# Kernel tuning notes

Hardware: AMD Instinct MI355X
Metric: run time of the kernel (lower is better)

Reference implementation:

```python
import jax, jax.numpy as jnp
import numpy as np

N = 300000   # active voxels at level 1
P = 150000   # indice pairs per kernel offset
K = 27       # 3x3x3 submanifold kernel offsets
C = 32       # nPlanes[0] = m
M = N // 8   # output voxels after stride-2 downsample
P2 = N       # stride-conv pairs for downsample
EPS = 1e-4   # BatchNorm1d eps in Semantic


def setup_inputs() -> dict:
    key = jax.random.key(0)
    ks = jax.random.split(key, 8)
    feats = jax.random.normal(ks[0], (N, C), jnp.float32)
    xyz = jax.random.normal(ks[1], (N, 3), jnp.float32)
    batch = jax.random.randint(ks[2], (N,), 0, 4)
    pair_in = jax.random.randint(ks[3], (K, P), 0, N)
    pair_out = jax.random.randint(ks[4], (K, P), 0, N)
    valid = jax.random.bernoulli(ks[5], 0.9, (K, P))
    pair_in = jnp.where(valid, pair_in, -1)  # spconv pads unused pairs with -1
    ds_pair_in = jax.random.randint(ks[6], (P2,), 0, N)
    ds_pair_out = jax.random.randint(ks[7], (P2,), 0, M)
    kw = jax.random.split(jax.random.key(1), 2)
    std = 1.0 / np.sqrt(C * K)
    W1 = jax.random.normal(kw[0], (K, C, C), jnp.float32) * std
    W2 = jax.random.normal(kw[1], (K, C, C), jnp.float32) * std
    return dict(feats=feats, xyz=xyz, batch=batch, pair_in=pair_in,
                pair_out=pair_out, ds_pair_in=ds_pair_in,
                ds_pair_out=ds_pair_out, W1=W1, W2=W2)


def bn_relu(x):
    # BatchNorm1d in train mode with weight=1, bias=0 (set_bn_init), then ReLU
    mu = jnp.mean(x, axis=0)
    var = jnp.var(x, axis=0)
    return jax.nn.relu((x - mu) * jax.lax.rsqrt(var + EPS))


def submconv(x, W, pair_in, pair_out):
    # gather-GEMM-scatter submanifold conv: x [N,Ci], W [K,Ci,Co], pairs [K,P]
    valid = pair_in >= 0
    gath = x[jnp.where(valid, pair_in, 0)]                 # [K,P,Ci]
    contrib = jnp.einsum('kpc,kcd->kpd', gath, W)          # [K,P,Co]
    seg = jnp.where(valid, pair_out, N).reshape(-1)        # invalid -> dump slot N
    out = jax.ops.segment_sum(contrib.reshape(-1, W.shape[-1]), seg,
                              num_segments=N + 1)
    return out[:N]


def scatter_mean(vals, idx_in, idx_out, num_out):
    valid = idx_in >= 0
    v = vals[jnp.where(valid, idx_in, 0)]
    v = jnp.where(valid[:, None], v, 0.0) if v.ndim == 2 else jnp.where(valid, v, 0.0)
    seg = jnp.where(valid, idx_out, num_out)
    sums = jax.ops.segment_sum(v, seg, num_segments=num_out + 1)[:num_out]
    cnt = jax.ops.segment_sum(valid.astype(jnp.float32), seg,
                              num_segments=num_out + 1)[:num_out]
    cnt = jnp.maximum(cnt, 1.0)
    return sums / (cnt[:, None] if sums.ndim == 2 else cnt)


def reference(feats, xyz, batch, pair_in, pair_out, ds_pair_in, ds_pair_out, W1, W2):
    # ResidualBlock: norm->relu->subm3x3 -> norm->relu->subm3x3, identity add
    h = submconv(bn_relu(feats), W1, pair_in, pair_out)
    h = submconv(bn_relu(h), W2, pair_in, pair_out)
    out = h + feats
    # get_downsample_info: scatter_mean of xyz and batch over stride-conv pairs
    xyz_next = scatter_mean(xyz, ds_pair_in, ds_pair_out, M)
    batch_next = scatter_mean(batch.astype(jnp.float32), ds_pair_in, ds_pair_out, M)
    return out, xyz_next, batch_next
```

## Files before the change

### kernel.cpp

```cpp
#include <hip/hip_runtime.h>

#define BN_EPS 1e-4f
#define BKT_SH 8
#define NBUCK_MAX 2560
#define CBLK 1024
#define LDSCAP 4096
#define P3CAP 4096

typedef __attribute__((ext_vector_type(8))) short short8;
typedef __attribute__((ext_vector_type(4))) float f32x4;
typedef __attribute__((ext_vector_type(4))) float floatv4;
typedef unsigned int uint;

union U4S8 { uint4 u; short8 s; };

static __device__ __forceinline__ unsigned short f2bf(float f) {
    unsigned u = __float_as_uint(f);
    unsigned r = (u + 0x7FFFu + ((u >> 16) & 1u)) >> 16;
    return (unsigned short)r;
}

__global__ void stats_bf16(const ushort* __restrict__ x,
                           float* __restrict__ stats, int n8) {
    const int t = threadIdx.x;
    long idx = (long)blockIdx.x * 256 + t;
    const long stride = (long)gridDim.x * 256;
    float s[8] = {0}, q[8] = {0};
    const uint4* x8 = (const uint4*)x;
    for (long e = idx; e < n8; e += stride) {
        uint4 v = x8[e];
        uint w0 = v.x, w1 = v.y, w2 = v.z, w3 = v.w;
        float f0 = __uint_as_float(w0 << 16), f1 = __uint_as_float(w0 & 0xFFFF0000u);
        float f2 = __uint_as_float(w1 << 16), f3 = __uint_as_float(w1 & 0xFFFF0000u);
        float f4 = __uint_as_float(w2 << 16), f5 = __uint_as_float(w2 & 0xFFFF0000u);
        float f6 = __uint_as_float(w3 << 16), f7 = __uint_as_float(w3 & 0xFFFF0000u);
        s[0]+=f0; q[0]+=f0*f0; s[1]+=f1; q[1]+=f1*f1;
        s[2]+=f2; q[2]+=f2*f2; s[3]+=f3; q[3]+=f3*f3;
        s[4]+=f4; q[4]+=f4*f4; s[5]+=f5; q[5]+=f5*f5;
        s[6]+=f6; q[6]+=f6*f6; s[7]+=f7; q[7]+=f7*f7;
    }
    __shared__ float red[256][8];
#pragma unroll
    for (int j = 0; j < 8; ++j) red[t][j] = s[j];
    __syncthreads();
    if (t < 32) {
        float a = 0.f;
        const int grp = t >> 3, j = t & 7;
#pragma unroll
        for (int m = 0; m < 64; ++m) a += red[grp + 4 * m][j];
        atomicAdd(&stats[t], a);
    }
    __syncthreads();
#pragma unroll
    for (int j = 0; j < 8; ++j) red[t][j] = q[j];
    __syncthreads();
    if (t < 32) {
        float a = 0.f;
        const int grp = t >> 3, j = t & 7;
#pragma unroll
        for (int m = 0; m < 64; ++m) a += red[grp + 4 * m][j];
        atomicAdd(&stats[32 + t], a);
    }
}

__global__ void bnrelu_f32(const float* __restrict__ x,
                           const float* __restrict__ stats,
                           ushort* __restrict__ xb, int n8, int N) {
    int idx = blockIdx.x * 256 + threadIdx.x;
    if (idx >= n8) return;
    const int c0 = (idx & 3) * 8;
    const float invN = 1.0f / (float)N;
    floatv4 v0 = *(const floatv4*)(x + (size_t)idx * 8);
    floatv4 v1 = *(const floatv4*)(x + (size_t)idx * 8 + 4);
    uint r[8];
#pragma unroll
    for (int j = 0; j < 8; ++j) {
        const int c = c0 + j;
        float mu = stats[c] * invN;
        float var = stats[32 + c] * invN - mu * mu;
        float rs = rsqrtf(var + BN_EPS);
        float f = (j < 4) ? v0[j] : v1[j - 4];
        float xn = fmaxf((f - mu) * rs, 0.f);
        r[j] = (uint)f2bf(xn);
    }
    uint4 o;
    o.x = r[0] | (r[1] << 16); o.y = r[2] | (r[3] << 16);
    o.z = r[4] | (r[5] << 16); o.w = r[6] | (r[7] << 16);
    *(uint4*)(xb + (size_t)idx * 8) = o;
}

__global__ void bnrelu_bf16(const ushort* __restrict__ h,
                            const float* __restrict__ stats,
                            ushort* __restrict__ xb, int n8, int N) {
    int idx = blockIdx.x * 256 + threadIdx.x;
    if (idx >= n8) return;
    const int c0 = (idx & 3) * 8;
    const float invN = 1.0f / (float)N;
    uint4 v = *(const uint4*)(h + (size_t)idx * 8);
    uint w[4] = {v.x, v.y, v.z, v.w};
    uint r[8];
#pragma unroll
    for (int j = 0; j < 8; ++j) {
        const int c = c0 + j;
        float mu = stats[c] * invN;
        float var = stats[32 + c] * invN - mu * mu;
        float rs = rsqrtf(var + BN_EPS);
        uint bits = (j & 1) ? (w[j >> 1] & 0xFFFF0000u) : (w[j >> 1] << 16);
        float f = __uint_as_float(bits);
        float xn = fmaxf((f - mu) * rs, 0.f);
        r[j] = (uint)f2bf(xn);
    }
    uint4 o;
    o.x = r[0] | (r[1] << 16); o.y = r[2] | (r[3] << 16);
    o.z = r[4] | (r[5] << 16); o.w = r[6] | (r[7] << 16);
    *(uint4*)(xb + (size_t)idx * 8) = o;
}

__global__ void prep2(const float* __restrict__ W1, const float* __restrict__ W2,
                      ushort* __restrict__ Wt1, ushort* __restrict__ Wt2,
                      ushort* __restrict__ xb,
                      const float* __restrict__ xyz, const int* __restrict__ batch,
                      floatv4* __restrict__ xyzb, int N, int B0,
                      const float* __restrict__ feats, float* __restrict__ stats1,
                      int total4) {
    const int t = threadIdx.x;
    if ((int)blockIdx.x >= B0) {
        const int bid = blockIdx.x - B0;
        long idx = (long)bid * 256 + t;
        const long stride = 1024L * 256;
        float s[4] = {0.f, 0.f, 0.f, 0.f}, q[4] = {0.f, 0.f, 0.f, 0.f};
        const floatv4* x4 = (const floatv4*)feats;
        for (long e = idx; e < total4; e += stride) {
            floatv4 v = x4[e];
#pragma unroll
            for (int j = 0; j < 4; ++j) { s[j] += v[j]; q[j] += v[j] * v[j]; }
        }
        __shared__ float red[256][4];
#pragma unroll
        for (int j = 0; j < 4; ++j) red[t][j] = s[j];
        __syncthreads();
        if (t < 32) {
            float a = 0.f;
            const int grp = t >> 2, j = t & 3;
#pragma unroll
            for (int m = 0; m < 32; ++m) a += red[grp + 8 * m][j];
            atomicAdd(&stats1[t], a);
        }
        __syncthreads();
#pragma unroll
        for (int j = 0; j < 4; ++j) red[t][j] = q[j];
        __syncthreads();
        if (t < 32) {
            float a = 0.f;
            const int grp = t >> 2, j = t & 3;
#pragma unroll
            for (int m = 0; m < 32; ++m) a += red[grp + 8 * m][j];
            atomicAdd(&stats1[32 + t], a);
        }
        return;
    }
    int idx = blockIdx.x * 256 + t;
    if (idx < 27 * 1024) {
        int k = idx >> 10, r = idx & 1023, co = r >> 5, ci = r & 31;
        Wt1[(k << 10) + (co << 5) + ci] = f2bf(W1[(k << 10) + (ci << 5) + co]);
    } else if (idx < 2 * 27 * 1024) {
        int i2 = idx - 27 * 1024;
        int k = i2 >> 10, r = i2 & 1023, co = r >> 5, ci = r & 31;
        Wt2[(k << 10) + (co << 5) + ci] = f2bf(W2[(k << 10) + (ci << 5) + co]);
    } else if (idx < 2 * 27 * 1024 + 32) {
        xb[(size_t)N * 32 + (idx - 2 * 27 * 1024)] = 0;
    } else {
        int i = idx - (2 * 27 * 1024 + 32);
        if (i < N) {
            floatv4 v;
            v[0] = xyz[(size_t)i * 3 + 0];
            v[1] = xyz[(size_t)i * 3 + 1];
            v[2] = xyz[(size_t)i * 3 + 2];
            v[3] = (float)batch[i];
            xyzb[i] = v;
        }
    }
}


__global__ void p1_count2(const int* __restrict__ pinA, const int* __restrict__ poutA,
                          uint* __restrict__ cntmatA, int KPA, int chunkA, int nbuckA,
                          const int* __restrict__ pinB, const int* __restrict__ poutB,
                          uint* __restrict__ cntmatB, int KPB, int chunkB, int nbuckB) {
    __shared__ uint H[NBUCK_MAX];
    const int t = threadIdx.x;
    const bool isA = (blockIdx.x < CBLK);
    const int j = isA ? blockIdx.x : (blockIdx.x - CBLK);
    const int* pin = isA ? pinA : pinB;
    const int* pout = isA ? poutA : poutB;
    uint* cntmat = isA ? cntmatA : cntmatB;
    const int KP = isA ? KPA : KPB;
    const int chunk = isA ? chunkA : chunkB;
    const int nbuck = isA ? nbuckA : nbuckB;
    for (int i = t; i < nbuck; i += 256) H[i] = 0;
    __syncthreads();
    const int r0 = j * chunk;
    const int r1 = min(KP, r0 + chunk);
    for (int r = r0 + t; r < r1; r += 256)
        if (pin[r] >= 0) atomicAdd(&H[((uint)pout[r]) >> BKT_SH], 1u);
    __syncthreads();
    uint* row = cntmat + (size_t)j * nbuck;
    for (int i = t; i < nbuck; i += 256) row[i] = H[i];
}

__global__ void p2_colscan2(uint* __restrict__ cntmatA, uint* __restrict__ btotA,
                            int nbuckA, int nblkA,
                            uint* __restrict__ cntmatB, uint* __restrict__ btotB,
                            int nbuckB) {
    const bool isA = ((int)blockIdx.x < nblkA);
    const int blk = isA ? blockIdx.x : (blockIdx.x - nblkA);
    uint* cntmat = isA ? cntmatA : cntmatB;
    uint* btot = isA ? btotA : btotB;
    const int nbuck = isA ? nbuckA : nbuckB;
    const int tid = threadIdx.x;
    const int bi  = tid & 15;
    const int seg = tid >> 4;
    const int b   = blk * 16 + bi;
    const int rpseg = CBLK / 16;
    const bool valid = (b < nbuck);
    uint s = 0;
    if (valid) {
        for (int u = 0; u < rpseg; ++u)
            s += cntmat[(size_t)(seg * rpseg + u) * nbuck + b];
    }
    __shared__ uint ss[16][16];
    ss[seg][bi] = s;
    __syncthreads();
    uint pre = 0;
    for (int g = 0; g < seg; ++g) pre += ss[g][bi];
    if (valid && seg == 15) btot[b] = pre + s;
    if (valid) {
        uint run = pre;
        for (int u = 0; u < rpseg; ++u) {
            size_t idx = (size_t)(seg * rpseg + u) * nbuck + b;
            uint v = cntmat[idx];
            cntmat[idx] = run;
            run += v;
        }
    }
}

__global__ void p3_bucketscan2(const uint* __restrict__ btotA, uint* __restrict__ bbaseA,
                               uint* __restrict__ startsA, int nbuckA, int NA,
                               const uint* __restrict__ btotB, uint* __restrict__ bbaseB,
                               uint* __restrict__ startsB, int nbuckB, int NB) {
    const uint* btot; uint* bbase; uint* starts; int nbuck; int N;
    if (blockIdx.x == 0) { btot = btotA; bbase = bbaseA; starts = startsA; nbuck = nbuckA; N = NA; }
    else                 { btot = btotB; bbase = bbaseB; starts = startsB; nbuck = nbuckB; N = NB; }
    const int t = threadIdx.x;
    __shared__ uint part[256];
    uint loc[10]; uint s = 0;
#pragma unroll
    for (int u = 0; u < 10; ++u) {
        int i = t * 10 + u;
        loc[u] = (i < nbuck) ? btot[i] : 0;
        s += loc[u];
    }
    part[t] = s;
    __syncthreads();
    for (int off = 1; off < 256; off <<= 1) {
        uint y = (t >= off) ? part[t - off] : 0;
        __syncthreads();
        part[t] += y;
        __syncthreads();
    }
    uint run = part[t] - s;
#pragma unroll
    for (int u = 0; u < 10; ++u) {
        int i = t * 10 + u;
        if (i < nbuck) { bbase[i] = run; run += loc[u]; }
    }
    if (t == 255) { bbase[nbuck] = run; starts[N] = run; }
}

__global__ __launch_bounds__(256)
void p4_place2(const int* __restrict__ pinA, const int* __restrict__ poutA,
               const uint* __restrict__ cntmatA, const uint* __restrict__ bbaseA,
               uint* __restrict__ tmpA, int KPA, int PA, int chunkA, int nbuckA,
               const int* __restrict__ pinB, const int* __restrict__ poutB,
               const uint* __restrict__ cntmatB, const uint* __restrict__ bbaseB,
               uint* __restrict__ tmpB, int KPB, int PB, int chunkB, int nbuckB) {
    __shared__ uint recs[LDSCAP];
    __shared__ ushort bof[LDSCAP];
    __shared__ uint H[NBUCK_MAX + 1];
    __shared__ uint C[NBUCK_MAX];
    __shared__ uint part[256];
    const int t = threadIdx.x;
    const bool isA = (blockIdx.x < CBLK);
    const int j = isA ? blockIdx.x : (blockIdx.x - CBLK);
    const int* pin = isA ? pinA : pinB;
    const int* pout = isA ? poutA : poutB;
    const uint* cntmat = isA ? cntmatA : cntmatB;
    const uint* bbase = isA ? bbaseA : bbaseB;
    uint* tmp = isA ? tmpA : tmpB;
    const int KP = isA ? KPA : KPB;
    const int P = isA ? PA : PB;
    const int chunk = isA ? chunkA : chunkB;
    const int nbuck = isA ? nbuckA : nbuckB;
    for (int i = t; i < nbuck; i += 256) H[i] = 0;
    __syncthreads();
    const int r0 = j * chunk;
    const int r1 = min(KP, r0 + chunk);
    for (int r = r0 + t; r < r1; r += 256)
        if (pin[r] >= 0) atomicAdd(&H[((uint)pout[r]) >> BKT_SH], 1u);
    __syncthreads();
    uint loc[10]; uint s = 0;
#pragma unroll
    for (int u = 0; u < 10; ++u) {
        int i = t * 10 + u;
        loc[u] = (i < nbuck) ? H[i] : 0;
        s += loc[u];
    }
    __syncthreads();
    part[t] = s;
    __syncthreads();
    for (int off = 1; off < 256; off <<= 1) {
        uint y = (t >= off) ? part[t - off] : 0;
        __syncthreads();
        part[t] += y;
        __syncthreads();
    }
    uint run = part[t] - s;
#pragma unroll
    for (int u = 0; u < 10; ++u) {
        int i = t * 10 + u;
        if (i < nbuck) { uint c = loc[u]; H[i] = run; run += c; }
    }
    if (t == 255) H[nbuck] = run;
    __syncthreads();
    for (int i = t; i < nbuck; i += 256) C[i] = H[i];
    __syncthreads();
    for (int r = r0 + t; r < r1; r += 256) {
        int ii = pin[r];
        if (ii < 0) continue;
        uint po = (uint)pout[r];
        uint b = po >> BKT_SH;
        uint k = (uint)r / (uint)P;
        uint pos = atomicAdd(&C[b], 1u);
        recs[pos] = ((po & 255u) << 24) | (k << 19) | (uint)ii;
        bof[pos] = (ushort)b;
    }
    __syncthreads();
    const uint tot = H[nbuck];
    for (int i = t; i < nbuck; i += 256)
        C[i] = bbase[i] + cntmat[(size_t)j * nbuck + i] - H[i];
    __syncthreads();
    for (uint sdx = t; sdx < tot; sdx += 256) {
        uint b = (uint)bof[sdx];
        tmp[C[b] + sdx] = recs[sdx];
    }
}

__global__ void p5_fine2(const uint* tmpA, const uint* __restrict__ bbaseA,
                         uint* entriesA, uint* __restrict__ startsA, int NA, int nbuckA,
                         const uint* tmpB, const uint* __restrict__ bbaseB,
                         uint* entriesB, uint* __restrict__ startsB, int NB) {
    __shared__ uint recs[P3CAP];
    __shared__ uint cnt[256];
    __shared__ uint curl[256];
    const bool isA = ((int)blockIdx.x < nbuckA);
    const int b = isA ? blockIdx.x : (blockIdx.x - nbuckA);
    const uint* tmp = isA ? tmpA : tmpB;
    const uint* bbase = isA ? bbaseA : bbaseB;
    uint* entries = isA ? entriesA : entriesB;
    uint* starts = isA ? startsA : startsB;
    const int N = isA ? NA : NB;
    const int t = threadIdx.x;
    const uint e0 = bbase[b];
    uint nrec = bbase[b + 1] - e0;
    if (nrec > P3CAP) nrec = P3CAP;
    for (uint s = t; s < nrec; s += 256) recs[s] = tmp[e0 + s];
    cnt[t] = 0; curl[t] = 0;
    __syncthreads();
    for (uint s = t; s < nrec; s += 256) atomicAdd(&cnt[recs[s] >> 24], 1u);
    __syncthreads();
    uint orig = cnt[t];
    for (int off = 1; off < 256; off <<= 1) {
        uint y = (t >= off) ? cnt[t - off] : 0;
        __syncthreads();
        cnt[t] += y;
        __syncthreads();
    }
    cnt[t] -= orig;
    __syncthreads();
    const int o0 = b << BKT_SH;
    if (o0 + t < N) starts[o0 + t] = e0 + cnt[t];
    for (uint s = t; s < nrec; s += 256) {
        uint lo = recs[s] >> 24;
        uint idx = atomicAdd(&curl[lo], 1u);
        entries[e0 + cnt[lo] + idx] = recs[s] & 0x00FFFFFFu;
    }
}

__global__ void conv1_csr(const ushort* __restrict__ xb,
                          const ushort* __restrict__ Wt,
                          const uint* __restrict__ starts,
                          const uint* __restrict__ entries,
                          ushort* __restrict__ outb,
                          int N) {
    const int w  = threadIdx.x >> 6;
    const int l  = threadIdx.x & 63;
    const int m  = l & 15;
    const int iq = l >> 4;
    const int o0 = (blockIdx.x * 4 + w) * 16;

    __shared__ uint eld[4][384];
    if (o0 >= N) return;

    const uint s0 = starts[o0];
    const uint sm = starts[o0 + m];
    const uint se = starts[o0 + m + 1];
    uint total = starts[o0 + 16] - s0;
    if (total > 384) total = 384;
    for (uint t = l; t < total; t += 64)
        eld[w][t] = entries[s0 + t];
    asm volatile("s_waitcnt lgkmcnt(0) vmcnt(0)" ::: "memory");
    __builtin_amdgcn_sched_barrier(0);

    if (iq == 0) {
        const uint a = sm - s0, bnd = se - s0;
        for (uint i = a + 1; i < bnd; ++i) {
            uint key = eld[w][i];
            uint j = i;
            while (j > a && eld[w][j - 1] > key) { eld[w][j] = eld[w][j - 1]; --j; }
            eld[w][j] = key;
        }
    }
    asm volatile("s_waitcnt lgkmcnt(0)" ::: "memory");
    __builtin_amdgcn_sched_barrier(0);

    f32x4 c0 = {0.f, 0.f, 0.f, 0.f};
    f32x4 c1 = {0.f, 0.f, 0.f, 0.f};
    uint q = sm - s0;
    const uint e = se - s0;
    uint ent = (q < e) ? eld[w][q] : 0xFFFFFFFFu;

    for (int k = 0; k < 27; ++k) {
        const ushort* wk = Wt + (k << 10);
        U4S8 b0, b1;
        b0.u = *(const uint4*)(wk + m * 32 + iq * 8);
        b1.u = *(const uint4*)(wk + (m + 16) * 32 + iq * 8);
        float a0=0.f,a1=0.f,a2=0.f,a3=0.f,a4=0.f,a5=0.f,a6=0.f,a7=0.f;
        bool got = false;
        while ((ent >> 19) == (uint)k) {
            got = true;
            const uint pi = ent & 0x7FFFFu;
            uint4 v = *(const uint4*)(xb + (size_t)pi * 32 + iq * 8);
            a0 += __uint_as_float(v.x << 16);
            a1 += __uint_as_float(v.x & 0xFFFF0000u);
            a2 += __uint_as_float(v.y << 16);
            a3 += __uint_as_float(v.y & 0xFFFF0000u);
            a4 += __uint_as_float(v.z << 16);
            a5 += __uint_as_float(v.z & 0xFFFF0000u);
            a6 += __uint_as_float(v.w << 16);
            a7 += __uint_as_float(v.w & 0xFFFF0000u);
            ++q;
            ent = (q < e) ? eld[w][q] : 0xFFFFFFFFu;
        }
        if (__any(got)) {
            U4S8 af;
            asm volatile("v_cvt_pk_bf16_f32 %0, %1, %2" : "=v"(af.u.x) : "v"(a0), "v"(a1));
            asm volatile("v_cvt_pk_bf16_f32 %0, %1, %2" : "=v"(af.u.y) : "v"(a2), "v"(a3));
            asm volatile("v_cvt_pk_bf16_f32 %0, %1, %2" : "=v"(af.u.z) : "v"(a4), "v"(a5));
            asm volatile("v_cvt_pk_bf16_f32 %0, %1, %2" : "=v"(af.u.w) : "v"(a6), "v"(a7));
            c0 = __builtin_amdgcn_mfma_f32_16x16x32_bf16(af.s, b0.s, c0, 0, 0, 0);
            c1 = __builtin_amdgcn_mfma_f32_16x16x32_bf16(af.s, b1.s, c1, 0, 0, 0);
        }
    }

#pragma unroll
    for (int j = 0; j < 4; ++j) {
        const long ro = (long)(o0 + iq * 4 + j) * 32;
        outb[ro + m]      = f2bf(c0[j]);
        outb[ro + 16 + m] = f2bf(c1[j]);
    }
}

__global__ void conv2_fused(const ushort* __restrict__ xb,
                            const ushort* __restrict__ Wt,
                            const uint* __restrict__ starts,
                            const uint* __restrict__ entries,
                            const float* __restrict__ iden,
                            float* __restrict__ outf,
                            int N, int cblocks,
                            const floatv4* __restrict__ xyzb,
                            const uint* __restrict__ starts2,
                            const uint* __restrict__ entries2,
                            float* __restrict__ out_xyz,
                            float* __restrict__ out_batch, int M) {
    if ((int)blockIdx.x >= cblocks) {
        int o = (blockIdx.x - cblocks) * 256 + threadIdx.x;
        if (o >= M) return;
        const uint s = starts2[o], e = starts2[o + 1];
        float sx = 0.f, sy = 0.f, sz = 0.f, sb = 0.f;
        for (uint q = s; q < e; ++q) {
            uint i = entries2[q] & 0x00FFFFFFu;
            floatv4 v = xyzb[i];
            sx += v[0]; sy += v[1]; sz += v[2]; sb += v[3];
        }
        float c = fmaxf((float)(e - s), 1.0f);
        float inv = 1.0f / c;
        out_xyz[(long)o * 3 + 0] = sx * inv;
        out_xyz[(long)o * 3 + 1] = sy * inv;
        out_xyz[(long)o * 3 + 2] = sz * inv;
        out_batch[o] = sb * inv;
        return;
    }
    const int w  = threadIdx.x >> 6;
    const int l  = threadIdx.x & 63;
    const int m  = l & 15;
    const int iq = l >> 4;
    const int o0 = (blockIdx.x * 4 + w) * 16;

    __shared__ uint eld[4][384];
    if (o0 >= N) return;

    const uint s0 = starts[o0];
    const uint sm = starts[o0 + m];
    const uint se = starts[o0 + m + 1];
    uint total = starts[o0 + 16] - s0;
    if (total > 384) total = 384;
    for (uint t = l; t < total; t += 64)
        eld[w][t] = entries[s0 + t];
    asm volatile("s_waitcnt lgkmcnt(0) vmcnt(0)" ::: "memory");
    __builtin_amdgcn_sched_barrier(0);

    if (iq == 0) {
        const uint a = sm - s0, bnd = se - s0;
        for (uint i = a + 1; i < bnd; ++i) {
            uint key = eld[w][i];
            uint j = i;
            while (j > a && eld[w][j - 1] > key) { eld[w][j] = eld[w][j - 1]; --j; }
            eld[w][j] = key;
        }
    }
    asm volatile("s_waitcnt lgkmcnt(0)" ::: "memory");
    __builtin_amdgcn_sched_barrier(0);

    f32x4 c0 = {0.f, 0.f, 0.f, 0.f};
    f32x4 c1 = {0.f, 0.f, 0.f, 0.f};
    uint q = sm - s0;
    const uint e = se - s0;
    uint ent = (q < e) ? eld[w][q] : 0xFFFFFFFFu;

    for (int k = 0; k < 27; ++k) {
        const ushort* wk = Wt + (k << 10);
        U4S8 b0, b1;
        b0.u = *(const uint4*)(wk + m * 32 + iq * 8);
        b1.u = *(const uint4*)(wk + (m + 16) * 32 + iq * 8);
        float a0=0.f,a1=0.f,a2=0.f,a3=0.f,a4=0.f,a5=0.f,a6=0.f,a7=0.f;
        bool got = false;
        while ((ent >> 19) == (uint)k) {
            got = true;
            const uint pi = ent & 0x7FFFFu;
            uint4 v = *(const uint4*)(xb + (size_t)pi * 32 + iq * 8);
            a0 += __uint_as_float(v.x << 16);
            a1 += __uint_as_float(v.x & 0xFFFF0000u);
            a2 += __uint_as_float(v.y << 16);
            a3 += __uint_as_float(v.y & 0xFFFF0000u);
            a4 += __uint_as_float(v.z << 16);
            a5 += __uint_as_float(v.z & 0xFFFF0000u);
            a6 += __uint_as_float(v.w << 16);
            a7 += __uint_as_float(v.w & 0xFFFF0000u);
            ++q;
            ent = (q < e) ? eld[w][q] : 0xFFFFFFFFu;
        }
        if (__any(got)) {
            U4S8 af;
            asm volatile("v_cvt_pk_bf16_f32 %0, %1, %2" : "=v"(af.u.x) : "v"(a0), "v"(a1));
            asm volatile("v_cvt_pk_bf16_f32 %0, %1, %2" : "=v"(af.u.y) : "v"(a2), "v"(a3));
            asm volatile("v_cvt_pk_bf16_f32 %0, %1, %2" : "=v"(af.u.z) : "v"(a4), "v"(a5));
            asm volatile("v_cvt_pk_bf16_f32 %0, %1, %2" : "=v"(af.u.w) : "v"(a6), "v"(a7));
            c0 = __builtin_amdgcn_mfma_f32_16x16x32_bf16(af.s, b0.s, c0, 0, 0, 0);
            c1 = __builtin_amdgcn_mfma_f32_16x16x32_bf16(af.s, b1.s, c1, 0, 0, 0);
        }
    }

#pragma unroll
    for (int j = 0; j < 4; ++j) {
        const long ro = (long)(o0 + iq * 4 + j) * 32;
        outf[ro + m]      = c0[j] + iden[ro + m];
        outf[ro + 16 + m] = c1[j] + iden[ro + 16 + m];
    }
}

extern "C" void kernel_launch(void* const* d_in, const int* in_sizes, int n_in,
                              void* d_out, int out_size, void* d_ws, size_t ws_size,
                              hipStream_t stream) {
    const float* feats = (const float*)d_in[0];
    const float* xyz   = (const float*)d_in[1];
    const int*   batch = (const int*)d_in[2];
    const int*   pin   = (const int*)d_in[3];
    const int*   pout  = (const int*)d_in[4];
    const int*   dsin  = (const int*)d_in[5];
    const int*   dsout = (const int*)d_in[6];
    const float* W1    = (const float*)d_in[7];
    const float* W2    = (const float*)d_in[8];

    const int N   = in_sizes[0] / 32;
    const int K   = 27;
    const int P   = in_sizes[3] / K;
    const int KP  = K * P;
    const int P2n = in_sizes[5];
    const int M   = (out_size - N * 32) / 4;
    const int nbuck = (N + 255) >> BKT_SH;
    const int chunk = (KP + CBLK - 1) / CBLK;
    const int nbuck2 = (M + 255) >> BKT_SH;
    const int chunk2 = (P2n + CBLK - 1) / CBLK;

    auto align256 = [](size_t x) { return (x + 255) & ~(size_t)255; };
    char* base = (char*)d_ws;
    size_t off = 0;
    float* stats1 = (float*)(base + off); off += 256;
    float* stats2 = (float*)(base + off); off += 256;
    const size_t zero_end = off;
    uint* cntmat  = (uint*)(base + off);  off = align256(off + (size_t)CBLK * nbuck * 4);
    uint* btot    = (uint*)(base + off);  off = align256(off + (size_t)nbuck * 4);
    uint* bbase   = (uint*)(base + off);  off = align256(off + (size_t)(nbuck + 1) * 4);
    uint* starts  = (uint*)(base + off);  off = align256(off + (size_t)(N + 1) * 4);
    uint* tmp     = (uint*)(base + off);  off = align256(off + (size_t)KP * 4);
    uint* entries = tmp;
    uint* cntmat2 = (uint*)(base + off);  off = align256(off + (size_t)CBLK * nbuck2 * 4);
    uint* btot2   = (uint*)(base + off);  off = align256(off + (size_t)nbuck2 * 4);
    uint* bbase2  = (uint*)(base + off);  off = align256(off + (size_t)(nbuck2 + 1) * 4);
    uint* starts2 = (uint*)(base + off);  off = align256(off + (size_t)(M + 1) * 4);
    uint* tmp2    = (uint*)(base + off);  off = align256(off + (size_t)P2n * 4);
    uint* entries2 = tmp2;
    ushort* Wt1   = (ushort*)(base + off); off = align256(off + 27 * 1024 * 2);
    ushort* Wt2   = (ushort*)(base + off); off = align256(off + 27 * 1024 * 2);
    ushort* xb    = (ushort*)(base + off); off = align256(off + (size_t)(N + 1) * 64);
    ushort* hacc  = (ushort*)(base + off); off = align256(off + (size_t)N * 64);
    floatv4* xyzb = (floatv4*)(base + off); off = align256(off + (size_t)N * 16);

    hipMemsetAsync(d_ws, 0, zero_end, stream);

    const int B0 = (2 * 27 * 1024 + 32 + N + 255) / 256;
    prep2<<<B0 + 1024, 256, 0, stream>>>(W1, W2, Wt1, Wt2, xb, xyz, batch, xyzb,
                                         N, B0, feats, stats1, N * 8);

    p1_count2<<<2 * CBLK, 256, 0, stream>>>(pin, pout, cntmat, KP, chunk, nbuck,
                                            dsin, dsout, cntmat2, P2n, chunk2, nbuck2);
    const int nblkA = (nbuck + 15) / 16, nblkB = (nbuck2 + 15) / 16;
    p2_colscan2<<<nblkA + nblkB, 256, 0, stream>>>(cntmat, btot, nbuck, nblkA,
                                                   cntmat2, btot2, nbuck2);
    p3_bucketscan2<<<2, 256, 0, stream>>>(btot, bbase, starts, nbuck, N,
                                          btot2, bbase2, starts2, nbuck2, M);
    p4_place2<<<2 * CBLK, 256, 0, stream>>>(pin, pout, cntmat, bbase, tmp, KP, P, chunk, nbuck,
                                            dsin, dsout, cntmat2, bbase2, tmp2, P2n, P2n, chunk2, nbuck2);
    p5_fine2<<<nbuck + nbuck2, 256, 0, stream>>>(tmp, bbase, entries, starts, N, nbuck,
                                                 tmp2, bbase2, entries2, starts2, M);

    bnrelu_f32<<<(N * 4 + 255) / 256, 256, 0, stream>>>(feats, stats1, xb, N * 4, N);
    const int cblocks = (N / 16 + 3) / 4;
    conv1_csr<<<cblocks, 256, 0, stream>>>(xb, Wt1, starts, entries, hacc, N);

    stats_bf16<<<1024, 256, 0, stream>>>(hacc, stats2, N * 4);
    bnrelu_bf16<<<(N * 4 + 255) / 256, 256, 0, stream>>>(hacc, stats2, xb, N * 4, N);
    float* out = (float*)d_out;
    const int dsblocks = (M + 255) / 256;
    conv2_fused<<<cblocks + dsblocks, 256, 0, stream>>>(
        xb, Wt2, starts, entries, feats, out, N, cblocks,
        xyzb, starts2, entries2,
        out + (size_t)N * 32, out + (size_t)N * 32 + (size_t)3 * M, M);
}
```

Baseline: 433.5 us.

## Fuse BN-ReLU of input into count kernel and sort CSR entries per output

The standalone bnrelu_f32 launch is removed and its work is folded into extra blocks of p1_count2, which saves one kernel launch and lets the BN pass overlap with the histogram counting. The fine bucketing in p5_fine2 now stages records in LDS and insertion-sorts each output's entry list by key before writing them out. Sorted entry lists should make the later gathers in the convolutions more coherent, but the per-thread insertion sort adds serial work in p5 and a second large LDS array that may lower occupancy.

After: 432.4 us. Within noise of the previous version (-0.2%).

```diff
diff --git a/kernel.cpp b/kernel.cpp
--- a/kernel.cpp
+++ b/kernel.cpp
@@ -61,32 +61,6 @@
         for (int m = 0; m < 64; ++m) a += red[grp + 4 * m][j];
         atomicAdd(&stats[32 + t], a);
     }
-}
-
-__global__ void bnrelu_f32(const float* __restrict__ x,
-                           const float* __restrict__ stats,
-                           ushort* __restrict__ xb, int n8, int N) {
-    int idx = blockIdx.x * 256 + threadIdx.x;
-    if (idx >= n8) return;
-    const int c0 = (idx & 3) * 8;
-    const float invN = 1.0f / (float)N;
-    floatv4 v0 = *(const floatv4*)(x + (size_t)idx * 8);
-    floatv4 v1 = *(const floatv4*)(x + (size_t)idx * 8 + 4);
-    uint r[8];
-#pragma unroll
-    for (int j = 0; j < 8; ++j) {
-        const int c = c0 + j;
-        float mu = stats[c] * invN;
-        float var = stats[32 + c] * invN - mu * mu;
-        float rs = rsqrtf(var + BN_EPS);
-        float f = (j < 4) ? v0[j] : v1[j - 4];
-        float xn = fmaxf((f - mu) * rs, 0.f);
-        r[j] = (uint)f2bf(xn);
-    }
-    uint4 o;
-    o.x = r[0] | (r[1] << 16); o.y = r[2] | (r[3] << 16);
-    o.z = r[4] | (r[5] << 16); o.w = r[6] | (r[7] << 16);
-    *(uint4*)(xb + (size_t)idx * 8) = o;
 }
 
 __global__ void bnrelu_bf16(const ushort* __restrict__ h,
@@ -186,9 +160,35 @@
 __global__ void p1_count2(const int* __restrict__ pinA, const int* __restrict__ poutA,
                           uint* __restrict__ cntmatA, int KPA, int chunkA, int nbuckA,
                           const int* __restrict__ pinB, const int* __restrict__ poutB,
-                          uint* __restrict__ cntmatB, int KPB, int chunkB, int nbuckB) {
+                          uint* __restrict__ cntmatB, int KPB, int chunkB, int nbuckB,
+                          const float* __restrict__ feats, const float* __restrict__ stats1,
+                          ushort* __restrict__ xb, int n8, int N) {
+    const int t = threadIdx.x;
+    if ((int)blockIdx.x >= 2 * CBLK) {
+        int idx = ((int)blockIdx.x - 2 * CBLK) * 256 + t;
+        if (idx >= n8) return;
+        const int c0 = (idx & 3) * 8;
+        const float invN = 1.0f / (float)N;
+        floatv4 v0 = *(const floatv4*)(feats + (size_t)idx * 8);
+        floatv4 v1 = *(const floatv4*)(feats + (size_t)idx * 8 + 4);
+        uint r[8];
+#pragma unroll
+        for (int j = 0; j < 8; ++j) {
+            const int c = c0 + j;
+            float mu = stats1[c] * invN;
+            float var = stats1[32 + c] * invN - mu * mu;
+            float rs = rsqrtf(var + BN_EPS);
+            float f = (j < 4) ? v0[j] : v1[j - 4];
+            float xn = fmaxf((f - mu) * rs, 0.f);
+            r[j] = (uint)f2bf(xn);
+        }
+        uint4 o;
+        o.x = r[0] | (r[1] << 16); o.y = r[2] | (r[3] << 16);
+        o.z = r[4] | (r[5] << 16); o.w = r[6] | (r[7] << 16);
+        *(uint4*)(xb + (size_t)idx * 8) = o;
+        return;
+    }
     __shared__ uint H[NBUCK_MAX];
-    const int t = threadIdx.x;
     const bool isA = (blockIdx.x < CBLK);
     const int j = isA ? blockIdx.x : (blockIdx.x - CBLK);
     const int* pin = isA ? pinA : pinB;
@@ -361,6 +361,7 @@
                          const uint* tmpB, const uint* __restrict__ bbaseB,
                          uint* entriesB, uint* __restrict__ startsB, int NB) {
     __shared__ uint recs[P3CAP];
+    __shared__ uint locs[P3CAP];
     __shared__ uint cnt[256];
     __shared__ uint curl[256];
     const bool isA = ((int)blockIdx.x < nbuckA);
@@ -393,8 +394,20 @@
     for (uint s = t; s < nrec; s += 256) {
         uint lo = recs[s] >> 24;
         uint idx = atomicAdd(&curl[lo], 1u);
-        entries[e0 + cnt[lo] + idx] = recs[s] & 0x00FFFFFFu;
-    }
+        locs[cnt[lo] + idx] = recs[s];
+    }
+    __syncthreads();
+    {
+        const uint a = cnt[t], bnd = a + curl[t];
+        for (uint i = a + 1; i < bnd; ++i) {
+            uint key = locs[i];
+            uint j2 = i;
+            while (j2 > a && locs[j2 - 1] > key) { locs[j2] = locs[j2 - 1]; --j2; }
+            locs[j2] = key;
+        }
+    }
+    __syncthreads();
+    for (uint s = t; s < nrec; s += 256) entries[e0 + s] = locs[s] & 0x00FFFFFFu;
 }
 
 __global__ void conv1_csr(const ushort* __restrict__ xb,
@@ -643,8 +656,11 @@
     prep2<<<B0 + 1024, 256, 0, stream>>>(W1, W2, Wt1, Wt2, xb, xyz, batch, xyzb,
                                          N, B0, feats, stats1, N * 8);
 
-    p1_count2<<<2 * CBLK, 256, 0, stream>>>(pin, pout, cntmat, KP, chunk, nbuck,
-                                            dsin, dsout, cntmat2, P2n, chunk2, nbuck2);
+    const int bnblk = (N * 4 + 255) / 256;
+    p1_count2<<<2 * CBLK + bnblk, 256, 0, stream>>>(
+        pin, pout, cntmat, KP, chunk, nbuck,
+        dsin, dsout, cntmat2, P2n, chunk2, nbuck2,
+        feats, stats1, xb, N * 4, N);
     const int nblkA = (nbuck + 15) / 16, nblkB = (nbuck2 + 15) / 16;
     p2_colscan2<<<nblkA + nblkB, 256, 0, stream>>>(cntmat, btot, nbuck, nblkA,
                                                    cntmat2, btot2, nbuck2);
@@ -655,7 +671,6 @@
     p5_fine2<<<nbuck + nbuck2, 256, 0, stream>>>(tmp, bbase, entries, starts, N, nbuck,
                                                  tmp2, bbase2, entries2, starts2, M);
 
-    bnrelu_f32<<<(N * 4 + 255) / 256, 256, 0, stream>>>(feats, stats1, xb, N * 4, N);
     const int cblocks = (N / 16 + 3) / 4;
     conv1_csr<<<cblocks, 256, 0, stream>>>(xb, Wt1, starts, entries, hacc, N);
 
```
